# Kernel optimization log

Measured on AMD Instinct MI355X. Metric: run time of the kernel, lower is better.

The kernel has to match this reference:

```python
import jax, jax.numpy as jnp
import numpy as np

H = 32  # GRU hidden size


def _conv1d(x, w, b, stride, pad):
    # x: (B, Cin, L), w: (Cout, Cin, K)
    y = jax.lax.conv_general_dilated(
        x, w, window_strides=(stride,), padding=[(pad, pad)],
        dimension_numbers=('NCH', 'OIH', 'NCH'))
    return y + b[None, :, None]


def setup_inputs() -> dict:
    key = jax.random.key(0)
    ks = jax.random.split(key, 16)
    B = 16384
    inp = {
        'past_samples': jax.random.normal(ks[0], (B, 2000), jnp.float32),
        'velocity': jax.random.uniform(ks[1], (B,), jnp.float32),
        'log_pitch': jax.random.normal(ks[2], (B,), jnp.float32),
        'time': jax.random.uniform(ks[3], (B,), jnp.float32),
        'hidden_state': jax.random.normal(ks[4], (B, H), jnp.float32),
        # conv stack params
        'w1': jax.random.normal(ks[5], (4, 1, 31), jnp.float32) * 0.1,
        'b1': jnp.zeros((4,), jnp.float32),
        'w2': jax.random.normal(ks[6], (8, 4, 15), jnp.float32) * 0.1,
        'b2': jnp.zeros((8,), jnp.float32),
        'w3': jax.random.normal(ks[7], (16, 8, 7), jnp.float32) * 0.1,
        'b3': jnp.zeros((16,), jnp.float32),
        # GRU params (torch layout: rows = [r; z; n])
        'w_ih': jax.random.normal(ks[8], (3 * H, 19), jnp.float32) * 0.1,
        'w_hh': jax.random.normal(ks[9], (3 * H, H), jnp.float32) * 0.1,
        'b_ih': jnp.zeros((3 * H,), jnp.float32),
        'b_hh': jnp.zeros((3 * H,), jnp.float32),
        # projection
        'w_proj': jax.random.normal(ks[10], (2, H), jnp.float32) * 0.1,
        'b_proj': jnp.zeros((2,), jnp.float32),
    }
    return inp


def reference(past_samples, velocity, log_pitch, time, hidden_state,
              w1, b1, w2, b2, w3, b3, w_ih, w_hh, b_ih, b_hh, w_proj, b_proj):
    x = past_samples[:, None, :]                       # (B,1,2000)
    x = jax.nn.relu(_conv1d(x, w1, b1, 4, 15))         # (B,4,500)
    x = jax.nn.relu(_conv1d(x, w2, b2, 4, 7))          # (B,8,125)
    x = jax.nn.relu(_conv1d(x, w3, b3, 4, 3))          # (B,16,32)
    ctx = jnp.mean(x, axis=2)                          # adaptive avg pool -> (B,16)

    rnn_in = jnp.concatenate(
        [ctx, velocity[:, None], log_pitch[:, None], time[:, None]], axis=1)  # (B,19)

    # single GRU step (torch GRUCell math)
    gi = rnn_in @ w_ih.T + b_ih                        # (B,3H)
    gh = hidden_state @ w_hh.T + b_hh                  # (B,3H)
    r = jax.nn.sigmoid(gi[:, :H] + gh[:, :H])
    z = jax.nn.sigmoid(gi[:, H:2 * H] + gh[:, H:2 * H])
    n = jnp.tanh(gi[:, 2 * H:] + r * gh[:, 2 * H:])
    new_hidden = (1.0 - z) * n + z * hidden_state      # (B,H)

    out = new_hidden @ w_proj.T + b_proj               # (B,2)
    mu, log_sigma = out[:, :1], out[:, 1:]
    sigma = jnp.exp(log_sigma)
    return (mu, sigma, new_hidden)
```

## Files before the change

### kernel.cpp

```cpp
#include <hip/hip_runtime.h>
#include <hip/hip_fp16.h>
#include <math.h>


typedef _Float16 h2 __attribute__((ext_vector_type(2)));
typedef _Float16 h4 __attribute__((ext_vector_type(4)));
typedef _Float16 h8 __attribute__((ext_vector_type(8)));
typedef float f4 __attribute__((ext_vector_type(4)));

__device__ __forceinline__ h8 ld_b8(const _Float16* p)
{
    h4 lo = *(const h4*)p;
    h4 hi = *(const h4*)(p + 4);
    return (h8){lo.x, lo.y, lo.z, lo.w, hi.x, hi.y, hi.z, hi.w};
}

__global__ void pack_weights(const float* __restrict__ w1,
                             const float* __restrict__ w2,
                             const float* __restrict__ w3,
                             const float* __restrict__ w_ih,
                             _Float16* __restrict__ hws,
                             float* __restrict__ wihp)
{
    for (int i = threadIdx.x; i < 512; i += 256) {
        int l = i >> 3, j = i & 7;
        int c = l & 15, k = ((l >> 4) << 3) + j;
        float v = (c < 4 && k >= 1) ? w1[c * 31 + (k - 1)] : 0.0f;
        hws[i] = (_Float16)v;
    }
    for (int i = threadIdx.x; i < 1024; i += 256) {
        int kk = i >> 9, l = (i >> 3) & 63, j = i & 7;
        int c = l & 15, k = kk * 32 + ((l >> 4) << 3) + j;
        int tap = k >> 2, ci = k & 3;
        float v = (c < 8 && tap < 15) ? w2[(c * 4 + ci) * 15 + tap] : 0.0f;
        hws[512 + i] = (_Float16)v;
    }
    for (int i = threadIdx.x; i < 1024; i += 256) {
        int kk = i >> 9, l = (i >> 3) & 63, j = i & 7;
        int c = l & 15, k = kk * 32 + ((l >> 4) << 3) + j;
        int tap = k >> 3, ci = k & 7;
        float v = (tap < 7) ? w3[(c * 8 + ci) * 7 + tap] : 0.0f;
        hws[1536 + i] = (_Float16)v;
    }
    for (int idx = threadIdx.x; idx < 96 * 20; idx += 256) {
        int r = idx / 20, c = idx % 20;
        wihp[idx] = (c < 19) ? w_ih[r * 19 + c] : 0.0f;
    }
}

__global__ void __launch_bounds__(64, 4)
wavernn_fused(const float* __restrict__ past,
              const float* __restrict__ velocity,
              const float* __restrict__ log_pitch,
              const float* __restrict__ time_in,
              const float* __restrict__ hidden,
              const float* __restrict__ b1,
              const float* __restrict__ b2,
              const float* __restrict__ b3,
              const float* __restrict__ wihp,
              const float* __restrict__ w_hh,
              const float* __restrict__ b_ih, const float* __restrict__ b_hh,
              const float* __restrict__ w_proj, const float* __restrict__ b_proj,
              const _Float16* __restrict__ hws,
              float* __restrict__ out, int B)
{
    __shared__ __align__(16) _Float16 X[2080];
    __shared__ __align__(16) _Float16 y1t[2080];
    __shared__ float rnn[20];
    __shared__ float hs[32];

    _Float16* const xbuf = X;
    _Float16* const y2t  = X;
    float* const gis     = (float*)X;
    float* const ghs     = (float*)X + 96;

    const h8* const wf1 = (const h8*)hws;
    const h8* const wf2 = (const h8*)(hws + 512);
    const h8* const wf3 = (const h8*)(hws + 1536);

    const int t = threadIdx.x;
    const int o = t >> 4;
    const int q = t & 15;
    const int b = blockIdx.x;

    const float4* row4 = (const float4*)(past + (size_t)b * 2000);

    if (t < 16) xbuf[t] = (_Float16)0.0f;
    xbuf[2016 + t] = (_Float16)0.0f;
    if (t < 28) y1t[t] = (_Float16)0.0f;
    if (t < 52) y1t[2028 + t] = (_Float16)0.0f;
    if (t < 32) hs[t] = hidden[(size_t)b * 32 + t];
    if (t == 0) rnn[16] = velocity[b];
    if (t == 1) rnn[17] = log_pitch[b];
    if (t == 2) rnn[18] = time_in[b];
    if (t == 3) rnn[19] = 0.0f;

#pragma unroll
    for (int j = 0; j < 8; ++j) {
        int i = t + 64 * j;
        if (i < 500) {
            float4 v = row4[i];
            h4 hv = {(_Float16)v.x, (_Float16)v.y, (_Float16)v.z, (_Float16)v.w};
            *(h4*)(xbuf + 16 + 4 * i) = hv;
        }
    }
    __syncthreads();

    {
        const h8 a1 = wf1[t];
        const float bv0 = b1[0], bv1 = b1[1], bv2 = b1[2], bv3 = b1[3];
        const f4 z = {0.0f, 0.0f, 0.0f, 0.0f};
#pragma unroll
        for (int T = 0; T < 32; ++T) {
            const int p = T * 16 + q;
            h8 x = ld_b8(xbuf + 4 * p + 8 * o);
            f4 d = __builtin_amdgcn_mfma_f32_16x16x32_f16(a1, x, z, 0, 0, 0);
            if (o == 0 && p < 500) {
                h4 w = {(_Float16)fmaxf(d[0] + bv0, 0.0f),
                        (_Float16)fmaxf(d[1] + bv1, 0.0f),
                        (_Float16)fmaxf(d[2] + bv2, 0.0f),
                        (_Float16)fmaxf(d[3] + bv3, 0.0f)};
                *(h4*)(y1t + (7 + p) * 4) = w;
            }
        }
    }
    __syncthreads();

    if (t < 24) y2t[t] = (_Float16)0.0f;
    if (t < 32) y2t[1024 + t] = (_Float16)0.0f;
    {
        const h8 a20 = wf2[t];
        const h8 a21 = wf2[64 + t];
        float b2v[4];
#pragma unroll
        for (int r = 0; r < 4; ++r) b2v[r] = b2[(o * 4 + r) & 7];
        const f4 z = {0.0f, 0.0f, 0.0f, 0.0f};
#pragma unroll
        for (int T = 0; T < 8; ++T) {
            const int p = T * 16 + q;
            h8 x0 = *(const h8*)(y1t + 16 * p + 8 * o);
            h8 x1 = *(const h8*)(y1t + 16 * p + 32 + 8 * o);
            f4 d = __builtin_amdgcn_mfma_f32_16x16x32_f16(a20, x0, z, 0, 0, 0);
            d = __builtin_amdgcn_mfma_f32_16x16x32_f16(a21, x1, d, 0, 0, 0);
            if (o < 2 && p < 125) {
                h4 w = {(_Float16)fmaxf(d[0] + b2v[0], 0.0f),
                        (_Float16)fmaxf(d[1] + b2v[1], 0.0f),
                        (_Float16)fmaxf(d[2] + b2v[2], 0.0f),
                        (_Float16)fmaxf(d[3] + b2v[3], 0.0f)};
                *(h4*)(y2t + (3 + p) * 8 + o * 4) = w;
            }
        }
    }
    __syncthreads();

    {
        const h8 a30 = wf3[t];
        const h8 a31 = wf3[64 + t];
        float b3v[4];
#pragma unroll
        for (int r = 0; r < 4; ++r) b3v[r] = b3[o * 4 + r];
        const f4 z = {0.0f, 0.0f, 0.0f, 0.0f};
        h8 x00 = *(const h8*)(y2t + 32 * q + 8 * o);
        h8 x01 = *(const h8*)(y2t + 32 * q + 32 + 8 * o);
        h8 x10 = *(const h8*)(y2t + 32 * (16 + q) + 8 * o);
        h8 x11 = *(const h8*)(y2t + 32 * (16 + q) + 32 + 8 * o);
        f4 d0 = __builtin_amdgcn_mfma_f32_16x16x32_f16(a30, x00, z, 0, 0, 0);
        d0 = __builtin_amdgcn_mfma_f32_16x16x32_f16(a31, x01, d0, 0, 0, 0);
        f4 d1 = __builtin_amdgcn_mfma_f32_16x16x32_f16(a30, x10, z, 0, 0, 0);
        d1 = __builtin_amdgcn_mfma_f32_16x16x32_f16(a31, x11, d1, 0, 0, 0);
#pragma unroll
        for (int r = 0; r < 4; ++r) {
            float v = fmaxf(d0[r] + b3v[r], 0.0f) + fmaxf(d1[r] + b3v[r], 0.0f);
            v += __shfl_xor(v, 1); v += __shfl_xor(v, 2);
            v += __shfl_xor(v, 4); v += __shfl_xor(v, 8);
            if (q == 0) rnn[o * 4 + r] = v * (1.0f / 32.0f);
        }
    }
    __syncthreads();

    {
        float rv[20];
#pragma unroll
        for (int j = 0; j < 20; ++j) rv[j] = rnn[j];

        float a = b_ih[t];
        const float4* wr = (const float4*)(wihp + t * 20);
#pragma unroll
        for (int j = 0; j < 5; ++j) {
            float4 qv = wr[j];
            a += rv[4 * j] * qv.x + rv[4 * j + 1] * qv.y +
                 rv[4 * j + 2] * qv.z + rv[4 * j + 3] * qv.w;
        }
        gis[t] = a;
        if (t < 32) {
            float a2 = b_ih[64 + t];
            const float4* wr2 = (const float4*)(wihp + (64 + t) * 20);
#pragma unroll
            for (int j = 0; j < 5; ++j) {
                float4 qv = wr2[j];
                a2 += rv[4 * j] * qv.x + rv[4 * j + 1] * qv.y +
                      rv[4 * j + 2] * qv.z + rv[4 * j + 3] * qv.w;
            }
            gis[64 + t] = a2;
        }

        float hv[32];
#pragma unroll
        for (int j = 0; j < 32; ++j) hv[j] = hs[j];

        float g = b_hh[t];
        const float4* wh = (const float4*)(w_hh + t * 32);
#pragma unroll
        for (int j = 0; j < 8; ++j) {
            float4 qv = wh[j];
            g += hv[4 * j] * qv.x + hv[4 * j + 1] * qv.y +
                 hv[4 * j + 2] * qv.z + hv[4 * j + 3] * qv.w;
        }
        ghs[t] = g;
        if (t < 32) {
            float g2 = b_hh[64 + t];
            const float4* wh2 = (const float4*)(w_hh + (64 + t) * 32);
#pragma unroll
            for (int j = 0; j < 8; ++j) {
                float4 qv = wh2[j];
                g2 += hv[4 * j] * qv.x + hv[4 * j + 1] * qv.y +
                      hv[4 * j + 2] * qv.z + hv[4 * j + 3] * qv.w;
            }
            ghs[64 + t] = g2;
        }
    }
    __syncthreads();

    if (t < 32) {
        const int j = t;
        float r = 1.0f / (1.0f + expf(-(gis[j] + ghs[j])));
        float z = 1.0f / (1.0f + expf(-(gis[32 + j] + ghs[32 + j])));
        float n = tanhf(gis[64 + j] + r * ghs[64 + j]);
        float nh = (1.0f - z) * n + z * hs[j];
        out[(size_t)2 * B + (size_t)b * 32 + j] = nh;

        float p0 = nh * w_proj[j];
        float p1 = nh * w_proj[32 + j];
        p0 += __shfl_xor(p0, 16); p1 += __shfl_xor(p1, 16);
        p0 += __shfl_xor(p0, 8);  p1 += __shfl_xor(p1, 8);
        p0 += __shfl_xor(p0, 4);  p1 += __shfl_xor(p1, 4);
        p0 += __shfl_xor(p0, 2);  p1 += __shfl_xor(p1, 2);
        p0 += __shfl_xor(p0, 1);  p1 += __shfl_xor(p1, 1);
        if (j == 0) {
            out[b] = p0 + b_proj[0];
            out[B + b] = expf(p1 + b_proj[1]);
        }
    }
}

extern "C" void kernel_launch(void* const* d_in, const int* in_sizes, int n_in,
                              void* d_out, int out_size, void* d_ws, size_t ws_size,
                              hipStream_t stream)
{
    const float* past      = (const float*)d_in[0];
    const float* velocity  = (const float*)d_in[1];
    const float* log_pitch = (const float*)d_in[2];
    const float* time_in   = (const float*)d_in[3];
    const float* hidden    = (const float*)d_in[4];
    const float* w1  = (const float*)d_in[5];
    const float* b1  = (const float*)d_in[6];
    const float* w2  = (const float*)d_in[7];
    const float* b2  = (const float*)d_in[8];
    const float* w3  = (const float*)d_in[9];
    const float* b3  = (const float*)d_in[10];
    const float* wih = (const float*)d_in[11];
    const float* whh = (const float*)d_in[12];
    const float* bih = (const float*)d_in[13];
    const float* bhh = (const float*)d_in[14];
    const float* wpr = (const float*)d_in[15];
    const float* bpr = (const float*)d_in[16];

    const int B = in_sizes[0] / 2000;
    _Float16* hws = (_Float16*)d_ws;
    float* wihp = (float*)((char*)d_ws + 8192);

    pack_weights<<<dim3(1), dim3(256), 0, stream>>>(w1, w2, w3, wih, hws, wihp);

    wavernn_fused<<<dim3(B), dim3(64), 0, stream>>>(
        past, velocity, log_pitch, time_in, hidden,
        b1, b2, b3, wihp, whh, bih, bhh, wpr, bpr,
        (const _Float16*)hws, (float*)d_out, B);
}
```

Baseline: 266.7 us.

## Split conv1 into two halves overlapping global loads, widen MFMA K, drop barriers

Conv1 weights are repacked so each MFMA pair computes four output positions per lane group with K=64, so all 64 lanes produce useful outputs instead of only one quarter. The input row load is split in two halves: the second half's global loads are issued before the first half's conv1 MFMAs, overlapping memory latency with compute. Since the block is a single wave, __syncthreads is replaced by an lgkmcnt wait. The barrier replacement relies on single-wave execution and on the compiler not reordering LDS accesses across the inline asm.

```diff
diff --git a/kernel.cpp b/kernel.cpp
--- a/kernel.cpp
+++ b/kernel.cpp
@@ -8,11 +8,14 @@
 typedef _Float16 h8 __attribute__((ext_vector_type(8)));
 typedef float f4 __attribute__((ext_vector_type(4)));
 
-__device__ __forceinline__ h8 ld_b8(const _Float16* p)
-{
-    h4 lo = *(const h4*)p;
-    h4 hi = *(const h4*)(p + 4);
-    return (h8){lo.x, lo.y, lo.z, lo.w, hi.x, hi.y, hi.z, hi.w};
+__device__ __forceinline__ void wave_sync()
+{
+    asm volatile("s_waitcnt lgkmcnt(0)" ::: "memory");
+}
+
+__device__ __forceinline__ h4 cvt4(float4 q)
+{
+    return (h4){(_Float16)q.x, (_Float16)q.y, (_Float16)q.z, (_Float16)q.w};
 }
 
 __global__ void pack_weights(const float* __restrict__ w1,
@@ -22,10 +25,13 @@
                              _Float16* __restrict__ hws,
                              float* __restrict__ wihp)
 {
-    for (int i = threadIdx.x; i < 512; i += 256) {
-        int l = i >> 3, j = i & 7;
-        int c = l & 15, k = ((l >> 4) << 3) + j;
-        float v = (c < 4 && k >= 1) ? w1[c * 31 + (k - 1)] : 0.0f;
+    for (int i = threadIdx.x; i < 1024; i += 256) {
+        int kk = i >> 9, l = (i >> 3) & 63, j = i & 7;
+        int m = l & 15, oct = l >> 4;
+        int k = kk * 32 + oct * 8 + j;
+        int delta = m >> 2, c = m & 3;
+        int tap = k - 4 * delta - 1;
+        float v = (tap >= 0 && tap < 31) ? w1[c * 31 + tap] : 0.0f;
         hws[i] = (_Float16)v;
     }
     for (int i = threadIdx.x; i < 1024; i += 256) {
@@ -33,14 +39,14 @@
         int c = l & 15, k = kk * 32 + ((l >> 4) << 3) + j;
         int tap = k >> 2, ci = k & 3;
         float v = (c < 8 && tap < 15) ? w2[(c * 4 + ci) * 15 + tap] : 0.0f;
-        hws[512 + i] = (_Float16)v;
+        hws[1024 + i] = (_Float16)v;
     }
     for (int i = threadIdx.x; i < 1024; i += 256) {
         int kk = i >> 9, l = (i >> 3) & 63, j = i & 7;
         int c = l & 15, k = kk * 32 + ((l >> 4) << 3) + j;
         int tap = k >> 3, ci = k & 7;
         float v = (tap < 7) ? w3[(c * 8 + ci) * 7 + tap] : 0.0f;
-        hws[1536 + i] = (_Float16)v;
+        hws[2048 + i] = (_Float16)v;
     }
     for (int idx = threadIdx.x; idx < 96 * 20; idx += 256) {
         int r = idx / 20, c = idx % 20;
@@ -64,8 +70,8 @@
               const _Float16* __restrict__ hws,
               float* __restrict__ out, int B)
 {
-    __shared__ __align__(16) _Float16 X[2080];
-    __shared__ __align__(16) _Float16 y1t[2080];
+    __shared__ __align__(16) _Float16 X[2112];
+    __shared__ __align__(16) _Float16 y1t[2112];
     __shared__ float rnn[20];
     __shared__ float hs[32];
 
@@ -75,8 +81,8 @@
     float* const ghs     = (float*)X + 96;
 
     const h8* const wf1 = (const h8*)hws;
-    const h8* const wf2 = (const h8*)(hws + 512);
-    const h8* const wf3 = (const h8*)(hws + 1536);
+    const h8* const wf2 = (const h8*)(hws + 1024);
+    const h8* const wf3 = (const h8*)(hws + 2048);
 
     const int t = threadIdx.x;
     const int o = t >> 4;
@@ -87,8 +93,10 @@
 
     if (t < 16) xbuf[t] = (_Float16)0.0f;
     xbuf[2016 + t] = (_Float16)0.0f;
+    if (t < 32) xbuf[2080 + t] = (_Float16)0.0f;
     if (t < 28) y1t[t] = (_Float16)0.0f;
-    if (t < 52) y1t[2028 + t] = (_Float16)0.0f;
+    y1t[2028 + t] = (_Float16)0.0f;
+    if (t < 20) y1t[2092 + t] = (_Float16)0.0f;
     if (t < 32) hs[t] = hidden[(size_t)b * 32 + t];
     if (t == 0) rnn[16] = velocity[b];
     if (t == 1) rnn[17] = log_pitch[b];
@@ -96,35 +104,65 @@
     if (t == 3) rnn[19] = 0.0f;
 
 #pragma unroll
-    for (int j = 0; j < 8; ++j) {
+    for (int j = 0; j < 4; ++j) {
         int i = t + 64 * j;
-        if (i < 500) {
-            float4 v = row4[i];
-            h4 hv = {(_Float16)v.x, (_Float16)v.y, (_Float16)v.z, (_Float16)v.w};
-            *(h4*)(xbuf + 16 + 4 * i) = hv;
-        }
-    }
-    __syncthreads();
-
-    {
-        const h8 a1 = wf1[t];
-        const float bv0 = b1[0], bv1 = b1[1], bv2 = b1[2], bv3 = b1[3];
-        const f4 z = {0.0f, 0.0f, 0.0f, 0.0f};
-#pragma unroll
-        for (int T = 0; T < 32; ++T) {
-            const int p = T * 16 + q;
-            h8 x = ld_b8(xbuf + 4 * p + 8 * o);
-            f4 d = __builtin_amdgcn_mfma_f32_16x16x32_f16(a1, x, z, 0, 0, 0);
-            if (o == 0 && p < 500) {
-                h4 w = {(_Float16)fmaxf(d[0] + bv0, 0.0f),
-                        (_Float16)fmaxf(d[1] + bv1, 0.0f),
-                        (_Float16)fmaxf(d[2] + bv2, 0.0f),
-                        (_Float16)fmaxf(d[3] + bv3, 0.0f)};
-                *(h4*)(y1t + (7 + p) * 4) = w;
-            }
-        }
-    }
-    __syncthreads();
+        if (i < 250) *(h4*)(xbuf + 16 + 4 * i) = cvt4(row4[i]);
+    }
+
+    float4 qb0, qb1, qb2, qb3;
+    {
+        const int i0 = 250 + t;
+        qb0 = row4[i0];
+        qb1 = row4[i0 + 64];
+        qb2 = row4[i0 + 128];
+        const int i3 = (i0 + 192 < 500) ? i0 + 192 : 499;
+        qb3 = row4[i3];
+    }
+    wave_sync();
+
+    const h8 a10 = wf1[t];
+    const h8 a11 = wf1[64 + t];
+    const float bv0 = b1[0], bv1 = b1[1], bv2 = b1[2], bv3 = b1[3];
+    const f4 z4 = {0.0f, 0.0f, 0.0f, 0.0f};
+#pragma unroll
+    for (int T = 0; T < 3; ++T) {
+        h8 x0 = *(const h8*)(xbuf + 256 * T + 16 * q + 8 * o);
+        h8 x1 = *(const h8*)(xbuf + 256 * T + 16 * q + 32 + 8 * o);
+        f4 d = __builtin_amdgcn_mfma_f32_16x16x32_f16(a10, x0, z4, 0, 0, 0);
+        d = __builtin_amdgcn_mfma_f32_16x16x32_f16(a11, x1, d, 0, 0, 0);
+        const int p = 64 * T + 4 * q + o;
+        h4 w = {(_Float16)fmaxf(d[0] + bv0, 0.0f),
+                (_Float16)fmaxf(d[1] + bv1, 0.0f),
+                (_Float16)fmaxf(d[2] + bv2, 0.0f),
+                (_Float16)fmaxf(d[3] + bv3, 0.0f)};
+        *(h4*)(y1t + (7 + p) * 4) = w;
+    }
+
+    {
+        const int i0 = 250 + t;
+        *(h4*)(xbuf + 16 + 4 * i0)         = cvt4(qb0);
+        *(h4*)(xbuf + 16 + 4 * (i0 + 64))  = cvt4(qb1);
+        *(h4*)(xbuf + 16 + 4 * (i0 + 128)) = cvt4(qb2);
+        if (i0 + 192 < 500) *(h4*)(xbuf + 16 + 4 * (i0 + 192)) = cvt4(qb3);
+    }
+    wave_sync();
+
+#pragma unroll
+    for (int T = 3; T < 8; ++T) {
+        h8 x0 = *(const h8*)(xbuf + 256 * T + 16 * q + 8 * o);
+        h8 x1 = *(const h8*)(xbuf + 256 * T + 16 * q + 32 + 8 * o);
+        f4 d = __builtin_amdgcn_mfma_f32_16x16x32_f16(a10, x0, z4, 0, 0, 0);
+        d = __builtin_amdgcn_mfma_f32_16x16x32_f16(a11, x1, d, 0, 0, 0);
+        const int p = 64 * T + 4 * q + o;
+        if (p < 500) {
+            h4 w = {(_Float16)fmaxf(d[0] + bv0, 0.0f),
+                    (_Float16)fmaxf(d[1] + bv1, 0.0f),
+                    (_Float16)fmaxf(d[2] + bv2, 0.0f),
+                    (_Float16)fmaxf(d[3] + bv3, 0.0f)};
+            *(h4*)(y1t + (7 + p) * 4) = w;
+        }
+    }
+    wave_sync();
 
     if (t < 24) y2t[t] = (_Float16)0.0f;
     if (t < 32) y2t[1024 + t] = (_Float16)0.0f;
@@ -134,13 +172,12 @@
         float b2v[4];
 #pragma unroll
         for (int r = 0; r < 4; ++r) b2v[r] = b2[(o * 4 + r) & 7];
-        const f4 z = {0.0f, 0.0f, 0.0f, 0.0f};
 #pragma unroll
         for (int T = 0; T < 8; ++T) {
             const int p = T * 16 + q;
             h8 x0 = *(const h8*)(y1t + 16 * p + 8 * o);
             h8 x1 = *(const h8*)(y1t + 16 * p + 32 + 8 * o);
-            f4 d = __builtin_amdgcn_mfma_f32_16x16x32_f16(a20, x0, z, 0, 0, 0);
+            f4 d = __builtin_amdgcn_mfma_f32_16x16x32_f16(a20, x0, z4, 0, 0, 0);
             d = __builtin_amdgcn_mfma_f32_16x16x32_f16(a21, x1, d, 0, 0, 0);
             if (o < 2 && p < 125) {
                 h4 w = {(_Float16)fmaxf(d[0] + b2v[0], 0.0f),
@@ -151,7 +188,7 @@
             }
         }
     }
-    __syncthreads();
+    wave_sync();
 
     {
         const h8 a30 = wf3[t];
@@ -159,14 +196,13 @@
         float b3v[4];
 #pragma unroll
         for (int r = 0; r < 4; ++r) b3v[r] = b3[o * 4 + r];
-        const f4 z = {0.0f, 0.0f, 0.0f, 0.0f};
         h8 x00 = *(const h8*)(y2t + 32 * q + 8 * o);
         h8 x01 = *(const h8*)(y2t + 32 * q + 32 + 8 * o);
         h8 x10 = *(const h8*)(y2t + 32 * (16 + q) + 8 * o);
         h8 x11 = *(const h8*)(y2t + 32 * (16 + q) + 32 + 8 * o);
-        f4 d0 = __builtin_amdgcn_mfma_f32_16x16x32_f16(a30, x00, z, 0, 0, 0);
+        f4 d0 = __builtin_amdgcn_mfma_f32_16x16x32_f16(a30, x00, z4, 0, 0, 0);
         d0 = __builtin_amdgcn_mfma_f32_16x16x32_f16(a31, x01, d0, 0, 0, 0);
-        f4 d1 = __builtin_amdgcn_mfma_f32_16x16x32_f16(a30, x10, z, 0, 0, 0);
+        f4 d1 = __builtin_amdgcn_mfma_f32_16x16x32_f16(a30, x10, z4, 0, 0, 0);
         d1 = __builtin_amdgcn_mfma_f32_16x16x32_f16(a31, x11, d1, 0, 0, 0);
 #pragma unroll
         for (int r = 0; r < 4; ++r) {
@@ -176,7 +212,7 @@
             if (q == 0) rnn[o * 4 + r] = v * (1.0f / 32.0f);
         }
     }
-    __syncthreads();
+    wave_sync();
 
     {
         float rv[20];
@@ -229,7 +265,7 @@
             ghs[64 + t] = g2;
         }
     }
-    __syncthreads();
+    wave_sync();
 
     if (t < 32) {
         const int j = t;
```

New measurement: 253.7 us. -4.9%, faster.
